# Kernel tuning notes

Hardware: AMD Instinct MI355X
Metric: run time of the kernel (lower is better)

Reference implementation:

```python
import jax, jax.numpy as jnp
import numpy as np

CONF_THRES = 0.4
IOU_THRES = 0.45
MAX_DET = 1000
MAX_WH = 7680.0  # class offset for non-agnostic NMS (yolov5 convention)
K = 2048         # pre-NMS candidate cap (>= MAX_DET)


def setup_inputs() -> dict:
    key = jax.random.key(0)
    k1, k2, k3, k4 = jax.random.split(key, 4)
    # uint8-valued image, stored as int32 (values 0..255)
    img = jax.random.randint(k1, (640, 640, 3), 0, 256, dtype=jnp.int32)
    B, N, NC = 8, 25200, 80
    xy = jax.random.uniform(k2, (B, N, 2)) * 640.0          # box centers in pixels
    wh = jax.random.uniform(k3, (B, N, 2)) * 80.0 + 4.0     # box sizes
    sc = jax.random.uniform(k4, (B, N, 1 + NC))             # objectness + class scores
    pred = jnp.concatenate([xy, wh, sc], axis=-1)           # [B, N, 85]
    return {"img": img, "pred": pred}


def _xywh2xyxy(x):
    xy, wh = x[..., :2], x[..., 2:4]
    return jnp.concatenate([xy - wh * 0.5, xy + wh * 0.5], axis=-1)


def _box_iou(a, b):
    # a: [K,4], b: [K,4] in xyxy
    lt = jnp.maximum(a[:, None, :2], b[None, :, :2])
    rb = jnp.minimum(a[:, None, 2:], b[None, :, 2:])
    wh = jnp.clip(rb - lt, 0.0)
    inter = wh[..., 0] * wh[..., 1]
    area_a = (a[:, 2] - a[:, 0]) * (a[:, 3] - a[:, 1])
    area_b = (b[:, 2] - b[:, 0]) * (b[:, 3] - b[:, 1])
    return inter / (area_a[:, None] + area_b[None, :] - inter + 1e-7)


def _nms_single(p):
    # p: [N, 5+nc]
    boxes = _xywh2xyxy(p[:, :4])                 # [N,4]
    conf_all = p[:, 5:] * p[:, 4:5]              # obj * cls
    conf = jnp.max(conf_all, axis=-1)            # best-class confidence [N]
    cls = jnp.argmax(conf_all, axis=-1).astype(p.dtype)
    scores = jnp.where(conf > CONF_THRES, conf, -1.0)
    # top-K candidates (score-sorted, padding gets score -1)
    top_s, idx = jax.lax.top_k(scores, K)
    b = boxes[idx]                               # [K,4] raw boxes
    c = cls[idx]                                 # [K] class ids (float)
    b_off = b + (c * MAX_WH)[:, None]            # class-offset boxes (agnostic_nms=False)
    iou = _box_iou(b_off, b_off)                 # [K,K]
    keep = top_s > CONF_THRES
    ar = jnp.arange(K)

    def body(i, keep):
        sup = keep[i] & (iou[i] > IOU_THRES) & (ar > i)
        return keep & jnp.logical_not(sup)

    keep = jax.lax.fori_loop(0, K, body, keep)
    fs = jnp.where(keep, top_s, -1.0)
    sel_s, sel = jax.lax.top_k(fs, MAX_DET)
    det = jnp.concatenate([b[sel], sel_s[:, None], c[sel][:, None]], axis=-1)  # [MAX_DET,6]
    return jnp.where((sel_s > CONF_THRES)[:, None], det, 0.0)


def reference(img, pred):
    # process_image: HWC -> CHW, BGR->RGB flip, float, /255, add batch dim
    x = img.astype(jnp.float32).transpose(2, 0, 1)[::-1] / 255.0
    x = x[None]                                  # [1,3,640,640]
    det = jax.vmap(_nms_single)(pred)[0]         # non_max_suppression(pred, ...)[0]
    return det, x
```

## Files before the change

kernel.cpp:

```cpp
#include <hip/hip_runtime.h>
#include <stdint.h>

#define N_ANCH 25200
#define NCLS   80
#define KSEL   2048
#define MAXDET 1000
#define CONF_T 0.4f
#define IOU_T  0.45f
#define MAX_WH 7680.0f
#define HBINS  512
#define HBASE  0xBE00u
#define NCAND_MAX 4096
#define NSB    788
#define NIB    1200
#define SUPCAP 224

#define WS_SELSCORE  0
#define WS_SELBOX    8192
#define WS_DETCAND   40960
#define WS_HIST      90112
#define WS_CNT       92160
#define WS_ANYSUP    92224
#define WS_KEYS      92480
#define WS_CLS       193280
#define WS_MASK      294912
#define WS_CAND      294912

__global__ void __launch_bounds__(256)
prep_kernel(const float* __restrict__ pred0, const int* __restrict__ img,
            float* __restrict__ xout, uint32_t* __restrict__ keys,
            int* __restrict__ cls, uint32_t* __restrict__ ghist) {
    int blk = blockIdx.x;
    int tid = threadIdx.x;
    if (blk < NSB) {
        int lane = tid & 63, wave = tid >> 6;
        int g = lane >> 3, l = lane & 7;
        int a = blk * 32 + wave * 8 + g;
        if (a >= N_ANCH) return;
        const float* p = pred0 + (size_t)a * 85;
        float obj = p[4];
        float v = -1e30f; int ci = 0;
        #pragma unroll
        for (int k = 0; k < 10; ++k) {
            int c = l + 8 * k;
            float x = p[5 + c] * obj;
            if (x > v) { v = x; ci = c; }
        }
        #pragma unroll
        for (int m = 1; m < 8; m <<= 1) {
            float ov = __shfl_xor(v, m, 64);
            int   oc = __shfl_xor(ci, m, 64);
            if (ov > v || (ov == v && oc < ci)) { v = ov; ci = oc; }
        }
        if (l == 0) {
            float score = (v > CONF_T) ? v : -1.0f;
            uint32_t bits = __float_as_uint(score);
            uint32_t key = (bits & 0x80000000u) ? ~bits : (bits | 0x80000000u);
            keys[a] = key; cls[a] = ci;
            if (key >= (HBASE << 16)) atomicAdd(&ghist[(key >> 16) - HBASE], 1u);
        }
    } else {
        int b = blk - NSB;
        int i4  = b * 1024 + tid * 4;
        int c   = i4 / 409600;
        int rem = i4 - c * 409600;
        int ch  = 2 - c;
        const int4* im4 = (const int4*)(img + (size_t)rem * 3);
        int4 v0 = im4[0], v1 = im4[1], v2 = im4[2];
        int p0 = (ch == 0) ? v0.x : (ch == 1) ? v0.y : v0.z;
        int p1 = (ch == 0) ? v0.w : (ch == 1) ? v1.x : v1.y;
        int p2 = (ch == 0) ? v1.z : (ch == 1) ? v1.w : v2.x;
        int p3 = (ch == 0) ? v2.y : (ch == 1) ? v2.z : v2.w;
        float4 o;
        o.x = (float)p0 / 255.0f; o.y = (float)p1 / 255.0f;
        o.z = (float)p2 / 255.0f; o.w = (float)p3 / 255.0f;
        *(float4*)(xout + i4) = o;
    }
}

__global__ void __launch_bounds__(256)
compact_kernel(const uint32_t* __restrict__ keys, const uint32_t* __restrict__ ghist,
               uint32_t* __restrict__ cnt, unsigned long long* __restrict__ cand) {
    __shared__ uint32_t h[HBINS];
    __shared__ uint32_t s_lim;
    __shared__ int wtot[4];
    __shared__ int s_base;
    int tid = threadIdx.x;
    int lane = tid & 63, wv = tid >> 6;

    h[tid] = ghist[tid]; h[tid + 256] = ghist[tid + 256];
    if (tid == 0) s_lim = (HBASE << 16);
    __syncthreads();
    for (int off = 1; off < HBINS; off <<= 1) {
        uint32_t a0 = h[tid] + ((tid + off < HBINS) ? h[tid + off] : 0u);
        uint32_t a1 = h[tid + 256] + ((tid + 256 + off < HBINS) ? h[tid + 256 + off] : 0u);
        __syncthreads();
        h[tid] = a0; h[tid + 256] = a1;
        __syncthreads();
    }
    for (int b = tid; b < HBINS; b += 256) {
        uint32_t sb  = h[b];
        uint32_t sb1 = (b < HBINS - 1) ? h[b + 1] : 0u;
        if (sb >= KSEL && sb1 < KSEL) s_lim = (uint32_t)(HBASE + b) << 16;
    }
    __syncthreads();
    uint32_t lim = s_lim;

    int i = blockIdx.x * 256 + tid;
    bool valid = (i < N_ANCH / 4);
    uint32_t ks[4] = {0, 0, 0, 0};
    int cm = 0;
    if (valid) {
        uint4 kk = ((const uint4*)keys)[i];
        ks[0] = kk.x; ks[1] = kk.y; ks[2] = kk.z; ks[3] = kk.w;
        #pragma unroll
        for (int j = 0; j < 4; ++j) cm += (ks[j] >= lim) ? 1 : 0;
    }
    int pre = cm;
    #pragma unroll
    for (int o = 1; o < 64; o <<= 1) {
        int v = __shfl_up(pre, o, 64);
        if (lane >= o) pre += v;
    }
    if (lane == 63) wtot[wv] = pre;
    __syncthreads();
    if (tid == 0) {
        int t = 0;
        #pragma unroll
        for (int w = 0; w < 4; ++w) { int x = wtot[w]; wtot[w] = t; t += x; }
        s_base = (t > 0) ? (int)atomicAdd(cnt, (uint32_t)t) : 0;
    }
    __syncthreads();
    int pos = s_base + wtot[wv] + (pre - cm);
    if (valid) {
        #pragma unroll
        for (int j = 0; j < 4; ++j) {
            if (ks[j] >= lim) {
                if (pos < NCAND_MAX)
                    cand[pos] = ((unsigned long long)ks[j] << 32)
                              | (uint32_t)(~(uint32_t)(i * 4 + j));
                ++pos;
            }
        }
    }
}

__global__ void __launch_bounds__(256)
rank_kernel(const uint32_t* __restrict__ cnt, const unsigned long long* __restrict__ cand,
            const float* __restrict__ pred0, const int* __restrict__ cls,
            float* __restrict__ sel_score, float4* __restrict__ selbox,
            float* __restrict__ det_cand) {
    __shared__ unsigned long long s_it[NCAND_MAX];
    __shared__ int s_n;
    int tid = threadIdx.x;
    if (tid == 0) s_n = (int)min(*cnt, (uint32_t)NCAND_MAX);
    __syncthreads();
    int n = s_n;
    int base = blockIdx.x * 32;
    if (base >= n) return;
    for (int i = tid; i < n; i += 256) s_it[i] = cand[i];
    __syncthreads();
    int grp = tid >> 4, s16 = tid & 15;
    #pragma unroll
    for (int o = 0; o < 2; ++o) {
        int it = base + grp + o * 16;
        if (it >= n) break;
        unsigned long long mine = s_it[it];
        int c = 0;
        for (int t = s16; t < n; t += 16)
            c += (s_it[t] > mine) ? 1 : 0;
        #pragma unroll
        for (int m = 1; m < 16; m <<= 1) c += __shfl_xor(c, m, 64);
        if (s16 == 0 && c < KSEL) {
            uint32_t key = (uint32_t)(mine >> 32);
            int ai = (int)(~(uint32_t)mine);
            uint32_t fb = (key & 0x80000000u) ? (key & 0x7FFFFFFFu) : ~key;
            float score = __uint_as_float(fb);
            const float* p = pred0 + (size_t)ai * 85;
            float x = p[0], y = p[1], w = p[2], hh = p[3];
            float x1 = x - w * 0.5f, y1 = y - hh * 0.5f;
            float x2 = x + w * 0.5f, y2 = y + hh * 0.5f;
            float cf = (float)cls[ai];
            float off = cf * MAX_WH;
            selbox[c] = make_float4(x1 + off, y1 + off, x2 + off, y2 + off);
            float* dc = det_cand + (size_t)c * 6;
            dc[0] = x1; dc[1] = y1; dc[2] = x2; dc[3] = y2; dc[4] = score; dc[5] = cf;
            sel_score[c] = score;
        }
    }
}

__global__ void __launch_bounds__(256)
mask_kernel(const float4* __restrict__ selbox, uint32_t* __restrict__ MT,
            uint32_t* __restrict__ anysup) {
    __shared__ float4 jb[32];
    int tid = threadIdx.x;
    int wi = blockIdx.x >> 3, rg = blockIdx.x & 7;

    if (tid < 32) jb[tid] = selbox[wi * 32 + tid];
    __syncthreads();
    int row = rg * 256 + tid;
    float4 a = selbox[row];
    float areaA = (a.z - a.x) * (a.w - a.y);
    uint32_t bits = 0;
    #pragma unroll 4
    for (int b = 0; b < 32; ++b) {
        int j = wi * 32 + b;
        if (j > row) {
            float4 q = jb[b];
            float lx = fmaxf(a.x, q.x), ly = fmaxf(a.y, q.y);
            float rx = fminf(a.z, q.z), ry = fminf(a.w, q.w);
            float ww = fmaxf(rx - lx, 0.0f), hh = fmaxf(ry - ly, 0.0f);
            float inter = ww * hh;
            float areaB = (q.z - q.x) * (q.w - q.y);
            float iou = inter / (areaA + areaB - inter + 1e-7f);
            if (iou > IOU_T) bits |= (1u << b);
        }
    }
    MT[(size_t)wi * 2048 + row] = bits;
    if (bits) atomicOr(&anysup[row >> 5], 1u << (row & 31));
}

__global__ void __launch_bounds__(256)
nms_kernel(const uint32_t* __restrict__ MT, const uint32_t* __restrict__ anysup,
           const float* __restrict__ sel_score,
           const float* __restrict__ det_cand, float* __restrict__ det) {
    __shared__ uint32_t f[64];
    __shared__ int rowlist[SUPCAP];
    __shared__ uint32_t sup[SUPCAP * 64];
    __shared__ int s_R;
    int tid = threadIdx.x;

    if (tid < 64) {
        uint32_t fw = anysup[tid];
        f[tid] = fw;
        int cnt = __popc(fw);
        int pre = cnt;
        for (int o = 1; o < 64; o <<= 1) {
            int v = __shfl_up(pre, o, 64);
            if (tid >= o) pre += v;
        }
        int r = pre - cnt;
        while (fw) {
            int b = __ffs(fw) - 1; fw &= fw - 1;
            if (r < SUPCAP) rowlist[r] = tid * 32 + b;
            ++r;
        }
        if (tid == 63) s_R = pre;
    }
    __syncthreads();
    int R = s_R;
    bool sparse = (R <= SUPCAP);
    if (sparse) {
        for (int s = tid >> 6; s < R; s += 4)
            sup[s * 64 + (tid & 63)] = MT[(size_t)(tid & 63) * 2048 + rowlist[s]];
    }
    __syncthreads();
    if (tid >= 64) return;

    int lane = tid;
    uint32_t removed = 0;
    #pragma unroll
    for (int b = 0; b < 32; ++b)
        if (!(sel_score[lane * 32 + b] > CONF_T)) removed |= (1u << b);

    if (sparse) {
        int slot = 0;
        for (int w = 0; w < 64; ++w) {
            uint32_t fb = f[w];
            while (fb) {
                int b = __ffs(fb) - 1; fb &= fb - 1;
                uint32_t rv = __shfl((int)removed, w, 64);
                if (!((rv >> b) & 1u))
                    removed |= sup[slot * 64 + lane];
                ++slot;
            }
        }
    } else {
        for (int c = 0; c < 64; ++c) {
            const uint4* mb = (const uint4*)(MT + (size_t)lane * 2048 + c * 32);
            uint4 qa[8];
            #pragma unroll
            for (int k = 0; k < 8; ++k) qa[k] = mb[k];
            uint32_t rw[32];
            #pragma unroll
            for (int k = 0; k < 8; ++k) {
                rw[4*k] = qa[k].x; rw[4*k+1] = qa[k].y;
                rw[4*k+2] = qa[k].z; rw[4*k+3] = qa[k].w;
            }
            uint32_t keptmask = 0;
            if (lane == c) {
                uint32_t myrem = removed;
                #pragma unroll
                for (int b = 0; b < 32; ++b)
                    if (!((myrem >> b) & 1u)) { keptmask |= (1u << b); myrem |= rw[b]; }
            }
            keptmask = __shfl(keptmask, c, 64);
            #pragma unroll
            for (int b = 0; b < 32; ++b)
                if ((keptmask >> b) & 1u) removed |= rw[b];
        }
    }

    uint32_t kw = ~removed;
    int cnt2 = __popc(kw);
    int pre = cnt2;
    for (int o = 1; o < 64; o <<= 1) {
        int v = __shfl_up(pre, o, 64);
        if (lane >= o) pre += v;
    }
    int excl = pre - cnt2;
    int total = __shfl(pre, 63, 64);

    int r = excl;
    for (int b = 0; b < 32; ++b) {
        if ((kw >> b) & 1u) {
            if (r < MAXDET) {
                const float* src = det_cand + (size_t)(lane * 32 + b) * 6;
                float* dst = det + (size_t)r * 6;
                for (int j = 0; j < 6; ++j) dst[j] = src[j];
            }
            ++r;
        }
    }
    int start = total < MAXDET ? total : MAXDET;
    for (int z = start + lane; z < MAXDET; z += 64) {
        float* dst = det + (size_t)z * 6;
        for (int j = 0; j < 6; ++j) dst[j] = 0.0f;
    }
}

extern "C" void kernel_launch(void* const* d_in, const int* in_sizes, int n_in,
                              void* d_out, int out_size, void* d_ws, size_t ws_size,
                              hipStream_t stream) {
    const int*   img  = (const int*)d_in[0];
    const float* pred = (const float*)d_in[1];
    float* out = (float*)d_out;
    char* ws = (char*)d_ws;

    float*    sel_score = (float*)(ws + WS_SELSCORE);
    float4*   selbox    = (float4*)(ws + WS_SELBOX);
    float*    det_cand  = (float*)(ws + WS_DETCAND);
    uint32_t* ghist     = (uint32_t*)(ws + WS_HIST);
    uint32_t* cnt       = (uint32_t*)(ws + WS_CNT);
    uint32_t* anysup    = (uint32_t*)(ws + WS_ANYSUP);
    uint32_t* keys      = (uint32_t*)(ws + WS_KEYS);
    int*      cls       = (int*)(ws + WS_CLS);
    uint32_t* MT        = (uint32_t*)(ws + WS_MASK);
    unsigned long long* cand = (unsigned long long*)(ws + WS_CAND);

    hipMemsetAsync(ghist, 0, 2368, stream);
    prep_kernel<<<NSB + NIB, 256, 0, stream>>>(pred, img, out + MAXDET * 6,
                                               keys, cls, ghist);
    compact_kernel<<<25, 256, 0, stream>>>(keys, ghist, cnt, cand);
    rank_kernel<<<128, 256, 0, stream>>>(cnt, cand, pred, cls,
                                         sel_score, selbox, det_cand);
    mask_kernel<<<512, 256, 0, stream>>>(selbox, MT, anysup);
    nms_kernel<<<1, 256, 0, stream>>>(MT, anysup, sel_score, det_cand, out);
}
```

Baseline: 164.8 us.

## Move image conversion into compact kernel and replace atomicOr flags with ballot writes

The image HWC->CHW normalization blocks move from the prep kernel into the launch of the compact kernel, so prep only does score reduction and the image work can fill the otherwise tiny 25-block compact launch. The mask kernel no longer issues atomicOr into a shared anysup bitmap. Each wave instead writes its own ballot mask into a per-tile flags array, which the NMS kernel ORs across 64 tiles. This removes the atomics and shrinks the memset, at the cost of 64 extra loads per thread in the single-block NMS kernel.

```diff
diff --git a/kernel.cpp b/kernel.cpp
--- a/kernel.cpp
+++ b/kernel.cpp
@@ -20,47 +20,56 @@
 #define WS_DETCAND   40960
 #define WS_HIST      90112
 #define WS_CNT       92160
-#define WS_ANYSUP    92224
 #define WS_KEYS      92480
 #define WS_CLS       193280
 #define WS_MASK      294912
+#define WS_FLAGS     819200
 #define WS_CAND      294912
 
 __global__ void __launch_bounds__(256)
-prep_kernel(const float* __restrict__ pred0, const int* __restrict__ img,
-            float* __restrict__ xout, uint32_t* __restrict__ keys,
+prep_kernel(const float* __restrict__ pred0, uint32_t* __restrict__ keys,
             int* __restrict__ cls, uint32_t* __restrict__ ghist) {
-    int blk = blockIdx.x;
-    int tid = threadIdx.x;
-    if (blk < NSB) {
-        int lane = tid & 63, wave = tid >> 6;
-        int g = lane >> 3, l = lane & 7;
-        int a = blk * 32 + wave * 8 + g;
-        if (a >= N_ANCH) return;
-        const float* p = pred0 + (size_t)a * 85;
-        float obj = p[4];
-        float v = -1e30f; int ci = 0;
-        #pragma unroll
-        for (int k = 0; k < 10; ++k) {
-            int c = l + 8 * k;
-            float x = p[5 + c] * obj;
-            if (x > v) { v = x; ci = c; }
-        }
-        #pragma unroll
-        for (int m = 1; m < 8; m <<= 1) {
-            float ov = __shfl_xor(v, m, 64);
-            int   oc = __shfl_xor(ci, m, 64);
-            if (ov > v || (ov == v && oc < ci)) { v = ov; ci = oc; }
-        }
-        if (l == 0) {
-            float score = (v > CONF_T) ? v : -1.0f;
-            uint32_t bits = __float_as_uint(score);
-            uint32_t key = (bits & 0x80000000u) ? ~bits : (bits | 0x80000000u);
-            keys[a] = key; cls[a] = ci;
-            if (key >= (HBASE << 16)) atomicAdd(&ghist[(key >> 16) - HBASE], 1u);
-        }
-    } else {
-        int b = blk - NSB;
+    int tid = threadIdx.x;
+    int lane = tid & 63, wave = tid >> 6;
+    int g = lane >> 3, l = lane & 7;
+    int a = blockIdx.x * 32 + wave * 8 + g;
+    if (a >= N_ANCH) return;
+    const float* p = pred0 + (size_t)a * 85;
+    float obj = p[4];
+    float v = -1e30f; int ci = 0;
+    #pragma unroll
+    for (int k = 0; k < 10; ++k) {
+        int c = l + 8 * k;
+        float x = p[5 + c] * obj;
+        if (x > v) { v = x; ci = c; }
+    }
+    #pragma unroll
+    for (int m = 1; m < 8; m <<= 1) {
+        float ov = __shfl_xor(v, m, 64);
+        int   oc = __shfl_xor(ci, m, 64);
+        if (ov > v || (ov == v && oc < ci)) { v = ov; ci = oc; }
+    }
+    if (l == 0) {
+        float score = (v > CONF_T) ? v : -1.0f;
+        uint32_t bits = __float_as_uint(score);
+        uint32_t key = (bits & 0x80000000u) ? ~bits : (bits | 0x80000000u);
+        keys[a] = key; cls[a] = ci;
+        if (key >= (HBASE << 16)) atomicAdd(&ghist[(key >> 16) - HBASE], 1u);
+    }
+}
+
+__global__ void __launch_bounds__(256)
+compact_kernel(const uint32_t* __restrict__ keys, const uint32_t* __restrict__ ghist,
+               uint32_t* __restrict__ cnt, unsigned long long* __restrict__ cand,
+               const int* __restrict__ img, float* __restrict__ xout) {
+    __shared__ uint32_t h[HBINS];
+    __shared__ uint32_t s_lim;
+    __shared__ int wtot[4];
+    __shared__ int s_base;
+    int tid = threadIdx.x;
+
+    if (blockIdx.x >= 25) {
+        int b = blockIdx.x - 25;
         int i4  = b * 1024 + tid * 4;
         int c   = i4 / 409600;
         int rem = i4 - c * 409600;
@@ -75,19 +84,10 @@
         o.x = (float)p0 / 255.0f; o.y = (float)p1 / 255.0f;
         o.z = (float)p2 / 255.0f; o.w = (float)p3 / 255.0f;
         *(float4*)(xout + i4) = o;
-    }
-}
-
-__global__ void __launch_bounds__(256)
-compact_kernel(const uint32_t* __restrict__ keys, const uint32_t* __restrict__ ghist,
-               uint32_t* __restrict__ cnt, unsigned long long* __restrict__ cand) {
-    __shared__ uint32_t h[HBINS];
-    __shared__ uint32_t s_lim;
-    __shared__ int wtot[4];
-    __shared__ int s_base;
-    int tid = threadIdx.x;
+        return;
+    }
+
     int lane = tid & 63, wv = tid >> 6;
-
     h[tid] = ghist[tid]; h[tid + 256] = ghist[tid + 256];
     if (tid == 0) s_lim = (HBASE << 16);
     __syncthreads();
@@ -192,9 +192,10 @@
 
 __global__ void __launch_bounds__(256)
 mask_kernel(const float4* __restrict__ selbox, uint32_t* __restrict__ MT,
-            uint32_t* __restrict__ anysup) {
+            uint32_t* __restrict__ flags) {
     __shared__ float4 jb[32];
     int tid = threadIdx.x;
+    int lane = tid & 63, wv = tid >> 6;
     int wi = blockIdx.x >> 3, rg = blockIdx.x & 7;
 
     if (tid < 32) jb[tid] = selbox[wi * 32 + tid];
@@ -218,11 +219,16 @@
         }
     }
     MT[(size_t)wi * 2048 + row] = bits;
-    if (bits) atomicOr(&anysup[row >> 5], 1u << (row & 31));
-}
-
-__global__ void __launch_bounds__(256)
-nms_kernel(const uint32_t* __restrict__ MT, const uint32_t* __restrict__ anysup,
+    unsigned long long bm = __ballot(bits != 0u);
+    if (lane == 0) {
+        int wbase = wi * 64 + rg * 8 + wv * 2;
+        flags[wbase]     = (uint32_t)bm;
+        flags[wbase + 1] = (uint32_t)(bm >> 32);
+    }
+}
+
+__global__ void __launch_bounds__(256)
+nms_kernel(const uint32_t* __restrict__ MT, const uint32_t* __restrict__ flags,
            const float* __restrict__ sel_score,
            const float* __restrict__ det_cand, float* __restrict__ det) {
     __shared__ uint32_t f[64];
@@ -232,7 +238,9 @@
     int tid = threadIdx.x;
 
     if (tid < 64) {
-        uint32_t fw = anysup[tid];
+        uint32_t fw = 0;
+        for (int wi = 0; wi < 64; ++wi)
+            fw |= flags[wi * 64 + tid];
         f[tid] = fw;
         int cnt = __popc(fw);
         int pre = cnt;
@@ -343,18 +351,18 @@
     float*    det_cand  = (float*)(ws + WS_DETCAND);
     uint32_t* ghist     = (uint32_t*)(ws + WS_HIST);
     uint32_t* cnt       = (uint32_t*)(ws + WS_CNT);
-    uint32_t* anysup    = (uint32_t*)(ws + WS_ANYSUP);
     uint32_t* keys      = (uint32_t*)(ws + WS_KEYS);
     int*      cls       = (int*)(ws + WS_CLS);
     uint32_t* MT        = (uint32_t*)(ws + WS_MASK);
+    uint32_t* flags     = (uint32_t*)(ws + WS_FLAGS);
     unsigned long long* cand = (unsigned long long*)(ws + WS_CAND);
 
-    hipMemsetAsync(ghist, 0, 2368, stream);
-    prep_kernel<<<NSB + NIB, 256, 0, stream>>>(pred, img, out + MAXDET * 6,
-                                               keys, cls, ghist);
-    compact_kernel<<<25, 256, 0, stream>>>(keys, ghist, cnt, cand);
+    hipMemsetAsync(ghist, 0, 2052, stream);
+    prep_kernel<<<NSB, 256, 0, stream>>>(pred, keys, cls, ghist);
+    compact_kernel<<<25 + NIB, 256, 0, stream>>>(keys, ghist, cnt, cand,
+                                                 img, out + MAXDET * 6);
     rank_kernel<<<128, 256, 0, stream>>>(cnt, cand, pred, cls,
                                          sel_score, selbox, det_cand);
-    mask_kernel<<<512, 256, 0, stream>>>(selbox, MT, anysup);
-    nms_kernel<<<1, 256, 0, stream>>>(MT, anysup, sel_score, det_cand, out);
-}
+    mask_kernel<<<512, 256, 0, stream>>>(selbox, MT, flags);
+    nms_kernel<<<1, 256, 0, stream>>>(MT, flags, sel_score, det_cand, out);
+}
```

Measured after the change: 164.7 us, median of 2. No clear change (-0.0%).
